# Kernel optimization log

Hardware: AMD Instinct MI355X
Metric: run time of the kernel (lower is better)

The kernel has to match this reference:

```python
import jax, jax.numpy as jnp
import numpy as np

N, G, D, F, A = 50000, 128, 32, 64, 8
N_ITERS, N_BLAYERS = 3, 3
EPS = 1e-5
HIN = D + F + 2 * F * A  # 1120: input to transform_out


def setup_inputs() -> dict:
    key = jax.random.key(0)
    ks = jax.random.split(key, 10)
    p = lambda k, shape: jax.random.normal(k, shape, jnp.float32) * 0.05
    return {
        "x": jax.random.normal(ks[0], (N, 3), jnp.float32),
        "batch": jnp.sort(jax.random.randint(ks[1], (N,), 0, G)),
        # input_network: Linear(3,D) + LayerNorm(D) + Tanh
        "Wi": p(ks[2], (3, D)), "bi": jnp.zeros((D,), jnp.float32),
        "lni_w": jnp.ones((D,), jnp.float32), "lni_b": jnp.zeros((D,), jnp.float32),
        # 3 BipartiteLayers (weights shared across graph iterations, stacked over layer idx)
        "W_in": p(ks[3], (N_BLAYERS, D, F)), "b_in": jnp.zeros((N_BLAYERS, F), jnp.float32),
        "W_sc": p(ks[4], (N_BLAYERS, F, A)), "b_sc": jnp.zeros((N_BLAYERS, A), jnp.float32),
        "W_out": p(ks[5], (N_BLAYERS, HIN, D)), "b_out": jnp.zeros((N_BLAYERS, D), jnp.float32),
        # PyG graph-mode LayerNorm after each BipartiteLayer
        "gln_w": jnp.ones((N_BLAYERS, D), jnp.float32), "gln_b": jnp.zeros((N_BLAYERS, D), jnp.float32),
        "Wp": p(ks[6], (3, D, D)), "bp": jnp.zeros((3, D), jnp.float32),
        "lnp_w": jnp.ones((3, D), jnp.float32), "lnp_b": jnp.zeros((3, D), jnp.float32),
        "Wpo": p(ks[7], (D, 1)), "bpo": jnp.zeros((1,), jnp.float32),
    }


def _ln(x, w, b):  # nn.LayerNorm over last dim
    m = x.mean(-1, keepdims=True)
    v = ((x - m) ** 2).mean(-1, keepdims=True)
    return (x - m) / jnp.sqrt(v + EPS) * w + b


def _graph_ln(x, w, b):  # PyG gnn.norm.LayerNorm, mode='graph', batch=None
    xc = x - x.mean()
    std = jnp.sqrt((xc * xc).mean())
    return xc / (std + EPS) * w + b


def _bipartite(x, batch, counts, Win, bin_, Wsc, bsc, Wout, bout):
    xp = x @ Win + bin_                                  # (N,F)
    attn = jnp.exp(-jnp.abs(xp @ Wsc + bsc))             # (N,A) 'potential' activation
    w = attn[:, :, None] * xp[:, None, :]                # (N,A,F) == einsum('nf,na->naf')
    sums = jax.ops.segment_sum(w, batch, num_segments=G)  # (G,A,F)
    cnt = counts[:, None, None]
    mean_p = sums / jnp.maximum(cnt, 1.0)
    max_p = jax.ops.segment_max(w, batch, num_segments=G)
    max_p = jnp.where(cnt > 0, max_p, 0.0)               # torch_scatter zero-fill for empty
    agg = jnp.concatenate([mean_p, max_p], axis=-1).reshape(G, 2 * F * A)  # (G,A,2F)->(G,2FA)
    H = jnp.concatenate([x, xp, agg[batch]], axis=-1)    # (N, HIN)
    return jnp.tanh(H @ Wout + bout)                     # Tanh hidden activation


def reference(x, batch, Wi, bi, lni_w, lni_b, W_in, b_in, W_sc, b_sc, W_out, b_out,
              gln_w, gln_b, Wp, bp, lnp_w, lnp_b, Wpo, bpo):
    counts = jax.ops.segment_sum(jnp.ones((x.shape[0],), x.dtype), batch, num_segments=G)
    h = jnp.tanh(_ln(x @ Wi + bi, lni_w, lni_b))
    for _ in range(N_ITERS):
        for j in range(N_BLAYERS):
            h = _bipartite(h, batch, counts, W_in[j], b_in[j], W_sc[j], b_sc[j], W_out[j], b_out[j])
            h = _graph_ln(h, gln_w[j], gln_b[j])
    s = jax.ops.segment_sum(h, batch, num_segments=G) / jnp.maximum(counts, 1.0)[:, None]  # scatter_mean
    for j in range(3):
        s = jnp.tanh(_ln(s @ Wp[j] + bp[j], lnp_w[j], lnp_b[j]))
    return (s @ Wpo + bpo).squeeze(-1)  # (G,)
```

## Files before the change

### kernel.cpp

```cpp
#include <hip/hip_runtime.h>
#include <math.h>

#define NPTS 50000
#define NG   128
#define DD   32
#define FF   64
#define AA   8
#define HINC 1120
#define EPSV 1e-5f
#define CH   64
#define NT   512

__device__ __forceinline__ float tanh_fast(float x) {
    float e = __expf(-2.f * fabsf(x));
    float r = __fdividef(1.f - e, 1.f + e);
    return copysignf(r, x);
}

__device__ __forceinline__ void embed4(const float* __restrict__ x,
                                       const float* __restrict__ Wi,
                                       const float* __restrict__ bi,
                                       const float* __restrict__ lniw,
                                       const float* __restrict__ lnib,
                                       int n, int d4,
                                       float& o0, float& o1, float& o2, float& o3) {
    float x0 = x[n*3], x1 = x[n*3+1], x2 = x[n*3+2];
    float tv0 = x0*Wi[d4+0] + x1*Wi[DD+d4+0] + x2*Wi[2*DD+d4+0] + bi[d4+0];
    float tv1 = x0*Wi[d4+1] + x1*Wi[DD+d4+1] + x2*Wi[2*DD+d4+1] + bi[d4+1];
    float tv2 = x0*Wi[d4+2] + x1*Wi[DD+d4+2] + x2*Wi[2*DD+d4+2] + bi[d4+2];
    float tv3 = x0*Wi[d4+3] + x1*Wi[DD+d4+3] + x2*Wi[2*DD+d4+3] + bi[d4+3];
    float sm = (tv0+tv1) + (tv2+tv3);
    sm += __shfl_xor(sm, 1); sm += __shfl_xor(sm, 2); sm += __shfl_xor(sm, 4);
    float mm = sm * (1.f/DD);
    float c0 = tv0-mm, c1 = tv1-mm, c2 = tv2-mm, c3 = tv3-mm;
    float qq = (c0*c0 + c1*c1) + (c2*c2 + c3*c3);
    qq += __shfl_xor(qq, 1); qq += __shfl_xor(qq, 2); qq += __shfl_xor(qq, 4);
    float inv = 1.f/sqrtf(qq*(1.f/DD) + EPSV);
    o0 = tanh_fast(c0*inv*lniw[d4+0] + lnib[d4+0]);
    o1 = tanh_fast(c1*inv*lniw[d4+1] + lnib[d4+1]);
    o2 = tanh_fast(c2*inv*lniw[d4+2] + lnib[d4+2]);
    o3 = tanh_fast(c3*inv*lniw[d4+3] + lnib[d4+3]);
}

__global__ __launch_bounds__(256) void k_setup(const int* __restrict__ batch,
                                               const float* __restrict__ W_in,
                                               const float* __restrict__ b_in,
                                               const float* __restrict__ W_out,
                                               const float* __restrict__ b_out,
                                               int* __restrict__ offs,
                                               float* __restrict__ stats,
                                               float* __restrict__ Weff,
                                               float* __restrict__ beff) {
    int t = threadIdx.x, bid = blockIdx.x;
    if (bid == 0) {
        if (t <= NG) {
            int lo = 0, hi = NPTS;
            while (lo < hi) { int mid = (lo+hi)>>1; if (batch[mid] < t) lo = mid+1; else hi = mid; }
            offs[t] = lo;
        }
        if (t < 32) stats[t] = 0.f;
    } else {
        int j = bid - 1;
        const float* W0 = W_out + (size_t)j*HINC*DD;
        const float* W1 = W0 + DD*DD;
        const float* Wi = W_in + (size_t)j*DD*FF;
        for (int e = t; e < DD*DD; e += 256) {
            int i = e >> 5, d = e & 31;
            float s = W0[e];
            for (int f = 0; f < FF; f++) s += Wi[i*FF+f] * W1[f*DD+d];
            Weff[j*DD*DD + e] = s;
        }
        if (t < DD) {
            float s = b_out[j*DD + t];
            for (int f = 0; f < FF; f++) s += b_in[j*FF+f] * W1[f*DD+t];
            beff[j*DD + t] = s;
        }
    }
}

__global__ __launch_bounds__(NT, 1) void k_L(const float* __restrict__ x,
                                             const float* __restrict__ Wi,
                                             const float* __restrict__ bi,
                                             const float* __restrict__ lniw,
                                             const float* __restrict__ lnib,
                                             const float* __restrict__ inb,
                                             const float* __restrict__ stats,
                                             const float* __restrict__ gw,
                                             const float* __restrict__ gb,
                                             const float* __restrict__ Win,
                                             const float* __restrict__ bin,
                                             const float* __restrict__ Wsc,
                                             const float* __restrict__ bsc,
                                             const int* __restrict__ offs,
                                             const float* __restrict__ Wagg,
                                             const float* __restrict__ beff,
                                             const float* __restrict__ Weff,
                                             float* __restrict__ tbuf,
                                             float* __restrict__ statsO,
                                             int isL0) {
    int g = blockIdx.x;
    int gs = offs[g], cnt = offs[g+1] - gs;
    const int t = threadIdx.x;
    if (cnt <= 0) return;

    __shared__ float sxp[2][CH][68];
    __shared__ float sattn[2][CH][9];
    __shared__ float sWin[DD*FF];
    __shared__ float sScT[AA*FF];
    __shared__ float sW[DD][36];
    __shared__ float agg[2*FF*AA];
    __shared__ float red[16][DD];
    __shared__ float aggWs[DD];
    __shared__ float sbin[FF];
    __shared__ float shW[DD];
    __shared__ float rs1[8], rs2[8];

    ((float4*)sWin)[t] = ((const float4*)Win)[t];
    { int a = t >> 6, f = t & 63; sScT[t] = Wsc[f*AA + a]; }
    for (int k = t; k < DD*DD; k += NT) sW[k >> 5][k & 31] = Weff[k];

    float gm = 0.f, ginv = 1.f;
    if (!isL0) {
        const float invM = 1.f/((float)NPTS*DD);
        gm = stats[0]*invM;
        float var = stats[1]*invM - gm*gm;
        ginv = 1.f/(sqrtf(fmaxf(var, 0.f)) + EPSV);
    }
    __syncthreads();
    if (!isL0) {
        if (t < FF) {
            float b = bin[t];
            for (int k = 0; k < DD; k++) {
                float sk = ginv * gw[k];
                float sh = gb[k] - gm * sk;
                b += sh * sWin[k*FF + t];
            }
            sbin[t] = b;
        } else if (t < FF + DD) {
            int d = t - FF;
            float r = 0.f;
            for (int k = 0; k < DD; k++) {
                float sk = ginv * gw[k];
                float sh = gb[k] - gm * sk;
                r += sh * sW[k][d];
            }
            shW[d] = r;
        }
        __syncthreads();
        for (int e = t; e < DD*FF; e += NT) sWin[e] *= ginv * gw[e >> 6];
        for (int e = t; e < DD*DD; e += NT) sW[e >> 5][e & 31] *= ginv * gw[e >> 5];
        __syncthreads();
    } else {
        if (t < FF) sbin[t] = bin[t];
        else if (t < FF + DD) shW[t - FF] = 0.f;
        __syncthreads();
    }

    const int pt = t >> 3, q = t & 7;
    const int fo = q * 8, d4 = q * 4;
    const int ca = t >> 6, cf = t & 63;
    const float bscv = bsc[q];
    const float4 bi0 = *(const float4*)&sbin[fo];
    const float4 bi1 = *(const float4*)&sbin[fo+4];
    float csum = 0.f, cmax = -INFINITY;

    float4 cur[8], nxt[8];
    {
        int np0 = min(CH, cnt);
        if (isL0) {
            if (pt < np0) {
                float o0,o1,o2,o3;
                embed4(x, Wi, bi, lniw, lnib, gs + pt, d4, o0,o1,o2,o3);
                #pragma unroll
                for (int j = 0; j < 8; j++) {
                    int src = (t & 56) | j;
                    cur[j].x = __shfl(o0, src, 64); cur[j].y = __shfl(o1, src, 64);
                    cur[j].z = __shfl(o2, src, 64); cur[j].w = __shfl(o3, src, 64);
                }
            }
        } else {
            int n0 = gs + min(pt, cnt-1);
            const float4* r4 = (const float4*)(inb + (size_t)n0*DD);
            #pragma unroll
            for (int j = 0; j < 8; j++) cur[j] = r4[j];
        }
    }
    int parity = 0;
    for (int base = gs; base < gs + cnt; base += CH, parity ^= 1) {
        int np = min(CH, gs + cnt - base);
        int nb = base + CH;
        if (nb < gs + cnt) {
            if (isL0) {
                int np1 = min(CH, gs + cnt - nb);
                if (pt < np1) {
                    float o0,o1,o2,o3;
                    embed4(x, Wi, bi, lniw, lnib, nb + pt, d4, o0,o1,o2,o3);
                    #pragma unroll
                    for (int j = 0; j < 8; j++) {
                        int src = (t & 56) | j;
                        nxt[j].x = __shfl(o0, src, 64); nxt[j].y = __shfl(o1, src, 64);
                        nxt[j].z = __shfl(o2, src, 64); nxt[j].w = __shfl(o3, src, 64);
                    }
                }
            } else {
                int nclamp = min(nb + pt, gs + cnt - 1);
                const float4* r4 = (const float4*)(inb + (size_t)nclamp*DD);
                #pragma unroll
                for (int j = 0; j < 8; j++) nxt[j] = r4[j];
            }
        }
        if (pt < np) {
            float xr[8] = {bi0.x,bi0.y,bi0.z,bi0.w,bi1.x,bi1.y,bi1.z,bi1.w};
            #pragma unroll
            for (int k4 = 0; k4 < 8; k4++) {
                float hv0 = cur[k4].x, hv1 = cur[k4].y, hv2 = cur[k4].z, hv3 = cur[k4].w;
                int kb = k4*4;
                float4 wa, wb;
                wa = *(const float4*)&sWin[(kb+0)*FF + fo]; wb = *(const float4*)&sWin[(kb+0)*FF + fo + 4];
                xr[0]+=hv0*wa.x; xr[1]+=hv0*wa.y; xr[2]+=hv0*wa.z; xr[3]+=hv0*wa.w;
                xr[4]+=hv0*wb.x; xr[5]+=hv0*wb.y; xr[6]+=hv0*wb.z; xr[7]+=hv0*wb.w;
                wa = *(const float4*)&sWin[(kb+1)*FF + fo]; wb = *(const float4*)&sWin[(kb+1)*FF + fo + 4];
                xr[0]+=hv1*wa.x; xr[1]+=hv1*wa.y; xr[2]+=hv1*wa.z; xr[3]+=hv1*wa.w;
                xr[4]+=hv1*wb.x; xr[5]+=hv1*wb.y; xr[6]+=hv1*wb.z; xr[7]+=hv1*wb.w;
                wa = *(const float4*)&sWin[(kb+2)*FF + fo]; wb = *(const float4*)&sWin[(kb+2)*FF + fo + 4];
                xr[0]+=hv2*wa.x; xr[1]+=hv2*wa.y; xr[2]+=hv2*wa.z; xr[3]+=hv2*wa.w;
                xr[4]+=hv2*wb.x; xr[5]+=hv2*wb.y; xr[6]+=hv2*wb.z; xr[7]+=hv2*wb.w;
                wa = *(const float4*)&sWin[(kb+3)*FF + fo]; wb = *(const float4*)&sWin[(kb+3)*FF + fo + 4];
                xr[0]+=hv3*wa.x; xr[1]+=hv3*wa.y; xr[2]+=hv3*wa.z; xr[3]+=hv3*wa.w;
                xr[4]+=hv3*wb.x; xr[5]+=hv3*wb.y; xr[6]+=hv3*wb.z; xr[7]+=hv3*wb.w;
            }
            float pa[8];
            #pragma unroll
            for (int a = 0; a < 8; a++) {
                float4 wa = *(const float4*)&sScT[a*FF + fo];
                float4 wb = *(const float4*)&sScT[a*FF + fo + 4];
                pa[a] = xr[0]*wa.x + xr[1]*wa.y + xr[2]*wa.z + xr[3]*wa.w
                      + xr[4]*wb.x + xr[5]*wb.y + xr[6]*wb.z + xr[7]*wb.w;
            }
            #pragma unroll
            for (int msk = 1; msk < 8; msk <<= 1) {
                #pragma unroll
                for (int a = 0; a < 8; a++) pa[a] += __shfl_xor(pa[a], msk);
            }
            sattn[parity][pt][q] = __expf(-fabsf(pa[q] + bscv));
            *(float4*)&sxp[parity][pt][fo]   = make_float4(xr[0],xr[1],xr[2],xr[3]);
            *(float4*)&sxp[parity][pt][fo+4] = make_float4(xr[4],xr[5],xr[6],xr[7]);
        }
        __syncthreads();
        #pragma unroll 4
        for (int pp = 0; pp < np; pp++) {
            float w = sattn[parity][pp][ca] * sxp[parity][pp][cf];
            csum += w; cmax = fmaxf(cmax, w);
        }
        #pragma unroll
        for (int j = 0; j < 8; j++) cur[j] = nxt[j];
    }

    __syncthreads();
    agg[ca*2*FF + cf]      = csum / (float)cnt;
    agg[ca*2*FF + FF + cf] = cmax;
    __syncthreads();
    {
        int d = t & 31, grp = t >> 5;
        float acc = 0.f;
        #pragma unroll
        for (int k2 = 0; k2 < 64; k2++) {
            int k = grp*64 + k2;
            acc += agg[k] * Wagg[k*DD + d];
        }
        red[grp][d] = acc;
    }
    __syncthreads();
    if (t < DD) {
        float r = 0.f;
        #pragma unroll
        for (int qq = 0; qq < 16; qq++) r += red[qq][t];
        aggWs[t] = r + beff[t] + shW[t];
    }
    __syncthreads();

    float s1 = 0.f, s2a = 0.f;
    if (pt < cnt) {
        float4 a0 = *(const float4*)&aggWs[d4];
        if (isL0) {
            for (int n = gs + pt; n < gs + cnt; n += CH) {
                float o0,o1,o2,o3;
                embed4(x, Wi, bi, lniw, lnib, n, d4, o0,o1,o2,o3);
                float4 row[8];
                #pragma unroll
                for (int j = 0; j < 8; j++) {
                    int src = (t & 56) | j;
                    row[j].x = __shfl(o0, src, 64); row[j].y = __shfl(o1, src, 64);
                    row[j].z = __shfl(o2, src, 64); row[j].w = __shfl(o3, src, 64);
                }
                float acc0 = a0.x, acc1 = a0.y, acc2 = a0.z, acc3 = a0.w;
                #pragma unroll
                for (int k4 = 0; k4 < 8; k4++) {
                    float hv0 = row[k4].x, hv1 = row[k4].y, hv2 = row[k4].z, hv3 = row[k4].w;
                    int kb = k4*4;
                    float4 w;
                    w = *(const float4*)&sW[kb+0][d4];
                    acc0 += hv0*w.x; acc1 += hv0*w.y; acc2 += hv0*w.z; acc3 += hv0*w.w;
                    w = *(const float4*)&sW[kb+1][d4];
                    acc0 += hv1*w.x; acc1 += hv1*w.y; acc2 += hv1*w.z; acc3 += hv1*w.w;
                    w = *(const float4*)&sW[kb+2][d4];
                    acc0 += hv2*w.x; acc1 += hv2*w.y; acc2 += hv2*w.z; acc3 += hv2*w.w;
                    w = *(const float4*)&sW[kb+3][d4];
                    acc0 += hv3*w.x; acc1 += hv3*w.y; acc2 += hv3*w.z; acc3 += hv3*w.w;
                }
                float4 o;
                o.x = tanh_fast(acc0); o.y = tanh_fast(acc1);
                o.z = tanh_fast(acc2); o.w = tanh_fast(acc3);
                *(float4*)&tbuf[(size_t)n*DD + d4] = o;
                s1  += (o.x + o.y) + (o.z + o.w);
                s2a += (o.x*o.x + o.y*o.y) + (o.z*o.z + o.w*o.w);
            }
        } else {
            float4 rcur[8], rnxt[8];
            {
                const float4* r4 = (const float4*)(inb + (size_t)(gs + pt)*DD);
                #pragma unroll
                for (int j = 0; j < 8; j++) rcur[j] = r4[j];
            }
            for (int n = gs + pt; n < gs + cnt; n += CH) {
                int nn = n + CH;
                int nclamp = (nn < gs + cnt) ? nn : n;
                {
                    const float4* r4 = (const float4*)(inb + (size_t)nclamp*DD);
                    #pragma unroll
                    for (int j = 0; j < 8; j++) rnxt[j] = r4[j];
                }
                float acc0 = a0.x, acc1 = a0.y, acc2 = a0.z, acc3 = a0.w;
                #pragma unroll
                for (int k4 = 0; k4 < 8; k4++) {
                    float hv0 = rcur[k4].x, hv1 = rcur[k4].y, hv2 = rcur[k4].z, hv3 = rcur[k4].w;
                    int kb = k4*4;
                    float4 w;
                    w = *(const float4*)&sW[kb+0][d4];
                    acc0 += hv0*w.x; acc1 += hv0*w.y; acc2 += hv0*w.z; acc3 += hv0*w.w;
                    w = *(const float4*)&sW[kb+1][d4];
                    acc0 += hv1*w.x; acc1 += hv1*w.y; acc2 += hv1*w.z; acc3 += hv1*w.w;
                    w = *(const float4*)&sW[kb+2][d4];
                    acc0 += hv2*w.x; acc1 += hv2*w.y; acc2 += hv2*w.z; acc3 += hv2*w.w;
                    w = *(const float4*)&sW[kb+3][d4];
                    acc0 += hv3*w.x; acc1 += hv3*w.y; acc2 += hv3*w.z; acc3 += hv3*w.w;
                }
                float4 o;
                o.x = tanh_fast(acc0); o.y = tanh_fast(acc1);
                o.z = tanh_fast(acc2); o.w = tanh_fast(acc3);
                *(float4*)&tbuf[(size_t)n*DD + d4] = o;
                s1  += (o.x + o.y) + (o.z + o.w);
                s2a += (o.x*o.x + o.y*o.y) + (o.z*o.z + o.w*o.w);
                #pragma unroll
                for (int j = 0; j < 8; j++) rcur[j] = rnxt[j];
            }
        }
    }
    #pragma unroll
    for (int o = 32; o > 0; o >>= 1) { s1 += __shfl_down(s1, o); s2a += __shfl_down(s2a, o); }
    int wid = t >> 6;
    __syncthreads();
    if ((t & 63) == 0) { rs1[wid] = s1; rs2[wid] = s2a; }
    __syncthreads();
    if (t == 0) {
        float a1 = 0.f, a2 = 0.f;
        #pragma unroll
        for (int qq = 0; qq < 8; qq++) { a1 += rs1[qq]; a2 += rs2[qq]; }
        atomicAdd(&statsO[0], a1);
        atomicAdd(&statsO[1], a2);
    }
}

__global__ __launch_bounds__(256) void k_read(const float* __restrict__ tbuf,
                                              const float* __restrict__ stats,
                                              const float* __restrict__ gw,
                                              const float* __restrict__ gb,
                                              const int* __restrict__ offs,
                                              const float* __restrict__ Wp,
                                              const float* __restrict__ bp,
                                              const float* __restrict__ lnw,
                                              const float* __restrict__ lnb,
                                              const float* __restrict__ Wpo,
                                              const float* __restrict__ bpo,
                                              float* __restrict__ out) {
    int g = blockIdx.x;
    int t = threadIdx.x;
    int d = t & 31, pl = t >> 5;
    int s0 = offs[g], e0 = offs[g+1];
    float acc = 0.f;
    for (int n = s0 + pl; n < e0; n += 8) acc += tbuf[(size_t)n*DD + d];
    __shared__ float red[8][DD];
    red[pl][d] = acc;
    __syncthreads();
    __shared__ float sv[DD];
    if (t < DD) {
        float r = 0.f;
        #pragma unroll
        for (int qq = 0; qq < 8; qq++) r += red[qq][t];
        const float invM = 1.f/((float)NPTS*DD);
        float m = stats[0]*invM;
        float var = stats[1]*invM - m*m;
        float inv = 1.f/(sqrtf(fmaxf(var, 0.f)) + EPSV);
        float cnt = (float)(e0 - s0);
        float mean = r / fmaxf(cnt, 1.f);
        sv[t] = (e0 > s0) ? (mean - m)*inv*gw[t] + gb[t] : 0.f;
    }
    __syncthreads();
    for (int j = 0; j < 3; j++) {
        float yv = 0.f;
        if (t < DD) {
            float y = bp[j*DD + t];
            #pragma unroll
            for (int i = 0; i < DD; i++) y += sv[i] * Wp[j*DD*DD + i*DD + t];
            float sum = y;
            #pragma unroll
            for (int o = 1; o < 32; o <<= 1) sum += __shfl_xor(sum, o);
            float m = sum * (1.f/DD);
            float c = y - m;
            float sq = c*c;
            #pragma unroll
            for (int o = 1; o < 32; o <<= 1) sq += __shfl_xor(sq, o);
            float var = sq * (1.f/DD);
            yv = tanh_fast(c / sqrtf(var + EPSV) * lnw[j*DD+t] + lnb[j*DD+t]);
        }
        __syncthreads();
        if (t < DD) sv[t] = yv;
        __syncthreads();
    }
    if (t < DD) {
        float p = sv[t] * Wpo[t];
        #pragma unroll
        for (int o = 1; o < 32; o <<= 1) p += __shfl_xor(p, o);
        if (t == 0) out[g] = p + bpo[0];
    }
}

extern "C" void kernel_launch(void* const* d_in, const int* in_sizes, int n_in,
                              void* d_out, int out_size, void* d_ws, size_t ws_size,
                              hipStream_t stream) {
    const float* x     = (const float*)d_in[0];
    const int*   batch = (const int*)  d_in[1];
    const float* Wi    = (const float*)d_in[2];
    const float* bi    = (const float*)d_in[3];
    const float* lni_w = (const float*)d_in[4];
    const float* lni_b = (const float*)d_in[5];
    const float* W_in  = (const float*)d_in[6];
    const float* b_in  = (const float*)d_in[7];
    const float* W_sc  = (const float*)d_in[8];
    const float* b_sc  = (const float*)d_in[9];
    const float* W_out = (const float*)d_in[10];
    const float* b_out = (const float*)d_in[11];
    const float* gln_w = (const float*)d_in[12];
    const float* gln_b = (const float*)d_in[13];
    const float* Wp    = (const float*)d_in[14];
    const float* bp    = (const float*)d_in[15];
    const float* lnp_w = (const float*)d_in[16];
    const float* lnp_b = (const float*)d_in[17];
    const float* Wpo   = (const float*)d_in[18];
    const float* bpo   = (const float*)d_in[19];
    float* out = (float*)d_out;

    float* ws    = (float*)d_ws;
    float* tbuf  = ws;
    float* stats = tbuf + (size_t)NPTS*DD;
    float* Weff  = stats + 32;
    float* beff  = Weff + 3*DD*DD;
    int*   offs  = (int*)(beff + 3*DD);

    k_setup<<<4, 256, 0, stream>>>(batch, W_in, b_in, W_out, b_out, offs, stats, Weff, beff);

    for (int L = 0; L < 9; ++L) {
        int j = L % 3;
        int pj = (L + 2) % 3;
        const float* st  = L ? stats + 2*(L-1) : nullptr;
        const float* pgw = L ? gln_w + pj*DD : nullptr;
        const float* pgb = L ? gln_b + pj*DD : nullptr;
        k_L<<<NG, NT, 0, stream>>>(
            x, Wi, bi, lni_w, lni_b,
            tbuf, st, pgw, pgb,
            W_in + (size_t)j*DD*FF, b_in + j*FF,
            W_sc + (size_t)j*FF*AA, b_sc + j*AA,
            offs,
            W_out + (size_t)j*HINC*DD + (size_t)96*DD, beff + j*DD,
            Weff + (size_t)j*DD*DD, tbuf, stats + 2*L, (L == 0) ? 1 : 0);
    }
    k_read<<<NG, 256, 0, stream>>>(tbuf, stats + 16, gln_w + 2*DD, gln_b + 2*DD,
                                   offs, Wp, bp, lnp_w, lnp_b, Wpo, bpo, out);
}
```

Before: 349.1 us.

## Accumulate attention-weighted mean/max pooling in registers instead of shared staging

Each thread now keeps 64 sum and 64 max register accumulators for its own 8 features times 8 attention heads, updated directly from the point it just projected. This removes the per-chunk shared-memory staging of projections and attention weights, and the block-wide barrier each chunk needed. Partial results are combined at the end with cross-lane shuffles, a per-wave shared stage, and one final cross-wave reduction. The cost is much higher register use, about 128 extra VGPRs, which risks spills or lower occupancy.

```diff
diff --git a/kernel.cpp b/kernel.cpp
--- a/kernel.cpp
+++ b/kernel.cpp
@@ -103,11 +103,11 @@
     const int t = threadIdx.x;
     if (cnt <= 0) return;
 
-    __shared__ float sxp[2][CH][68];
-    __shared__ float sattn[2][CH][9];
     __shared__ float sWin[DD*FF];
     __shared__ float sScT[AA*FF];
     __shared__ float sW[DD][36];
+    __shared__ float stageS[8][512];
+    __shared__ float stageM[8][512];
     __shared__ float agg[2*FF*AA];
     __shared__ float red[16][DD];
     __shared__ float aggWs[DD];
@@ -159,10 +159,15 @@
     const int pt = t >> 3, q = t & 7;
     const int fo = q * 8, d4 = q * 4;
     const int ca = t >> 6, cf = t & 63;
-    const float bscv = bsc[q];
     const float4 bi0 = *(const float4*)&sbin[fo];
     const float4 bi1 = *(const float4*)&sbin[fo+4];
-    float csum = 0.f, cmax = -INFINITY;
+    float bscr[8];
+    #pragma unroll
+    for (int a = 0; a < 8; a++) bscr[a] = bsc[a];
+
+    float asum[64], amax[64];
+    #pragma unroll
+    for (int i = 0; i < 64; i++) { asum[i] = 0.f; amax[i] = -INFINITY; }
 
     float4 cur[8], nxt[8];
     {
@@ -185,8 +190,7 @@
             for (int j = 0; j < 8; j++) cur[j] = r4[j];
         }
     }
-    int parity = 0;
-    for (int base = gs; base < gs + cnt; base += CH, parity ^= 1) {
+    for (int base = gs; base < gs + cnt; base += CH) {
         int np = min(CH, gs + cnt - base);
         int nb = base + CH;
         if (nb < gs + cnt) {
@@ -242,24 +246,56 @@
                 #pragma unroll
                 for (int a = 0; a < 8; a++) pa[a] += __shfl_xor(pa[a], msk);
             }
-            sattn[parity][pt][q] = __expf(-fabsf(pa[q] + bscv));
-            *(float4*)&sxp[parity][pt][fo]   = make_float4(xr[0],xr[1],xr[2],xr[3]);
-            *(float4*)&sxp[parity][pt][fo+4] = make_float4(xr[4],xr[5],xr[6],xr[7]);
-        }
-        __syncthreads();
-        #pragma unroll 4
-        for (int pp = 0; pp < np; pp++) {
-            float w = sattn[parity][pp][ca] * sxp[parity][pp][cf];
-            csum += w; cmax = fmaxf(cmax, w);
+            #pragma unroll
+            for (int a = 0; a < 8; a++) {
+                float atv = __expf(-fabsf(pa[a] + bscr[a]));
+                #pragma unroll
+                for (int j = 0; j < 8; j++) {
+                    float w = atv * xr[j];
+                    asum[a*8+j] += w;
+                    amax[a*8+j] = fmaxf(amax[a*8+j], w);
+                }
+            }
         }
         #pragma unroll
         for (int j = 0; j < 8; j++) cur[j] = nxt[j];
     }
 
-    __syncthreads();
-    agg[ca*2*FF + cf]      = csum / (float)cnt;
-    agg[ca*2*FF + FF + cf] = cmax;
-    __syncthreads();
+    #pragma unroll
+    for (int msk = 8; msk <= 32; msk <<= 1) {
+        #pragma unroll
+        for (int i = 0; i < 64; i++) {
+            asum[i] += __shfl_xor(asum[i], msk);
+            amax[i] = fmaxf(amax[i], __shfl_xor(amax[i], msk));
+        }
+    }
+    {
+        int wv = t >> 6;
+        if ((t & 56) == 0) {
+            int qq = t & 7;
+            #pragma unroll
+            for (int a = 0; a < 8; a++) {
+                #pragma unroll
+                for (int j = 0; j < 8; j++) {
+                    stageS[wv][a*FF + qq*8 + j] = asum[a*8+j];
+                    stageM[wv][a*FF + qq*8 + j] = amax[a*8+j];
+                }
+            }
+        }
+    }
+    __syncthreads();
+    {
+        float sum = 0.f, mx = -INFINITY;
+        #pragma unroll
+        for (int wv = 0; wv < 8; wv++) {
+            sum += stageS[wv][ca*FF + cf];
+            mx = fmaxf(mx, stageM[wv][ca*FF + cf]);
+        }
+        agg[ca*2*FF + cf]      = sum / (float)cnt;
+        agg[ca*2*FF + FF + cf] = mx;
+    }
+    __syncthreads();
+
     {
         int d = t & 31, grp = t >> 5;
         float acc = 0.f;
```

Measured after the change: 436.0 us. +24.9%, slower.
